# Kernel tuning notes

Hardware: AMD Instinct MI355X
Metric: run time of the kernel (lower is better)

The kernel has to match this reference:

```python
import jax, jax.numpy as jnp
import numpy as np

EPS = 1e-5

def _dw_conv_bn(x, w, gamma, beta):
    # depthwise 'same' conv: w is (C,1,k,k), feature_group_count = C
    C = x.shape[1]
    k = w.shape[-1]
    p = k // 2
    y = jax.lax.conv_general_dilated(
        x, w,
        window_strides=(1, 1),
        padding=((p, p), (p, p)),
        dimension_numbers=("NCHW", "OIHW", "NCHW"),
        feature_group_count=C,
    )
    # BatchNorm2d (training mode: batch stats over N,H,W per channel, biased var)
    mean = jnp.mean(y, axis=(0, 2, 3), keepdims=True)
    var = jnp.var(y, axis=(0, 2, 3), keepdims=True)
    inv = jax.lax.rsqrt(var + EPS)
    g = gamma.reshape(1, -1, 1, 1)
    b = beta.reshape(1, -1, 1, 1)
    return (y - mean) * inv * g + b


def setup_inputs() -> dict:
    key = jax.random.key(0)
    ks = jax.random.split(key, 3)
    B, C, H, W = 16, 384, 56, 56
    x = jax.random.normal(ks[0], (B, C, H, W), dtype=jnp.float32)
    w_large = jax.random.normal(ks[1], (C, 1, 31, 31), dtype=jnp.float32) * 0.02
    w_small = jax.random.normal(ks[2], (C, 1, 5, 5), dtype=jnp.float32) * 0.1
    gamma_large = jnp.ones((C,), dtype=jnp.float32)
    beta_large = jnp.zeros((C,), dtype=jnp.float32)
    gamma_small = jnp.ones((C,), dtype=jnp.float32)
    beta_small = jnp.zeros((C,), dtype=jnp.float32)
    return {
        "x": x,
        "w_large": w_large, "gamma_large": gamma_large, "beta_large": beta_large,
        "w_small": w_small, "gamma_small": gamma_small, "beta_small": beta_small,
    }


def reference(x, w_large, gamma_large, beta_large, w_small, gamma_small, beta_small):
    out = _dw_conv_bn(x, w_large, gamma_large, beta_large)
    out = out + _dw_conv_bn(x, w_small, gamma_small, beta_small)
    return out
```

## Files before the change

kernel.cpp:

```cpp
#include <hip/hip_runtime.h>
#include <hip/hip_bf16.h>

#define BB 16
#define CC 384
#define HH 56
#define WW 56
#define PLANE (HH*WW)
#define NHW (BB*PLANE)

typedef __attribute__((ext_vector_type(8)))  short short8;
typedef __attribute__((ext_vector_type(16))) float f32x16;
typedef __attribute__((ext_vector_type(4)))  unsigned int uint4v;
typedef __attribute__((ext_vector_type(4)))  float float4v;
typedef unsigned int uint;

#define PSTR 92
#define PROWS 86
#define PSZ (PROWS*PSTR)
#define WL_W 100
#define WS_W 80

static __device__ __forceinline__ short f2bf(float f) {
    unsigned int u = __float_as_uint(f);
    unsigned int r = (u + 0x7fffu + ((u >> 16) & 1u)) >> 16;
    return (short)r;
}

static __device__ __forceinline__ short8 ldA(const short* ap) {
    union { uint u[4]; short8 v; } r;
    uint2 lo = *(const uint2*)(ap);
    uint2 hi = *(const uint2*)(ap + 4);
    r.u[0] = lo.x; r.u[1] = lo.y; r.u[2] = hi.x; r.u[3] = hi.y;
    return r.v;
}

static __device__ __forceinline__ short8 ldW(const uint* p) {
    union { uint u[4]; short8 v; } r;
    r.u[0] = p[0]; r.u[1] = p[2]; r.u[2] = p[4]; r.u[3] = p[6];
    return r.v;
}

template<bool PACK>
__global__ __launch_bounds__(256)
__attribute__((amdgpu_waves_per_eu(3)))
void conv_large_k(
    const float* __restrict__ x, const float* __restrict__ wL,
    const float* __restrict__ wS,
    unsigned short* __restrict__ yL, uint* __restrict__ pk,
    float* __restrict__ stats)
{
    __shared__ __align__(16) short planes[2*PSZ];
    __shared__ __align__(16) uint  wpL[31*WL_W];
    __shared__ __align__(16) uint  wpS[5*WS_W];
    __shared__ float red_s[16];

    const int bid  = blockIdx.x;
    const int c    = bid % CC;
    const int pg   = bid / CC;
    const int tid  = threadIdx.x;
    const int w    = tid >> 6;
    const int p    = w >> 1;
    const int tx   = w & 1;
    const int lane = tid & 63;
    const int m    = lane & 31;
    const int g    = lane >> 5;

    {
        uint4 z = make_uint4(0,0,0,0);
        uint4* p4 = (uint4*)planes;
        #pragma unroll 1
        for (int i = tid; i < 2*PSZ/8; i += 256) p4[i] = z;
    }
    __syncthreads();

    short* pl = planes + p*PSZ;
    const int b = pg*2 + p;
    const float4* xp4 = (const float4*)(x + ((size_t)b*CC + c)*PLANE);
    #pragma unroll 1
    for (int i4 = lane + 64*tx; i4 < PLANE/4; i4 += 128) {
        float4 v = xp4[i4];
        int e  = 4*i4;
        int r  = e / WW;
        int cc = e - r*WW;
        short* dst = &pl[(r + 15)*PSTR + cc + 15];
        dst[0] = f2bf(v.x); dst[1] = f2bf(v.y); dst[2] = f2bf(v.z); dst[3] = f2bf(v.w);
    }

    const float* wrow = wL + c*961;
    #pragma unroll 1
    for (int i = tid; i < 31*WL_W; i += 256) {
        int ky = i / WL_W;
        int j  = i - ky*WL_W;
        int widx = j - 32;
        uint lo = (widx   >= 0 && widx   < 31) ? (uint)(unsigned short)f2bf(wrow[ky*31 + widx])     : 0u;
        uint hi = (widx+1 >= 0 && widx+1 < 31) ? (uint)(unsigned short)f2bf(wrow[ky*31 + widx + 1]) : 0u;
        wpL[i] = lo | (hi << 16);
    }
    const float* wrowS = wS + c*25;
    #pragma unroll 1
    for (int i = tid; i < 5*WS_W; i += 256) {
        int ky = i / WS_W;
        int j  = i - ky*WS_W;
        int widx = j - 32;
        uint lo = (widx   >= 0 && widx   < 5) ? (uint)(unsigned short)f2bf(wrowS[ky*5 + widx])     : 0u;
        uint hi = (widx+1 >= 0 && widx+1 < 5) ? (uint)(unsigned short)f2bf(wrowS[ky*5 + widx + 1]) : 0u;
        wpS[i] = lo | (hi << 16);
    }
    __syncthreads();

    const int  toff = 8*g - m;
    const uint* wLd = wpL + (toff + 32);
    const uint* wSd = wpS + (toff + 31);
    const short* abase = pl + m*PSTR + 8*g + tx*24;

    f32x16 acc[2] = {};

    short8 A0[8], B0[4], A1[8], B1[4];
    {
        #pragma unroll
        for (int s = 0; s < 4; ++s) B0[s] = ldW(wLd + 16*s);
        #pragma unroll
        for (int s = 0; s < 4; ++s) {
            A0[2*s]   = ldA(abase + 16*s);
            A0[2*s+1] = ldA(abase + 24*PSTR + 16*s);
        }
    }
    #pragma unroll 1
    for (int ky = 0; ky < 30; ky += 2) {
        {
            const uint* wk = wLd + (ky+1)*WL_W;
            const short* ar = abase + (ky+1)*PSTR;
            #pragma unroll
            for (int s = 0; s < 4; ++s) B1[s] = ldW(wk + 16*s);
            #pragma unroll
            for (int s = 0; s < 4; ++s) {
                A1[2*s]   = ldA(ar + 16*s);
                A1[2*s+1] = ldA(ar + 24*PSTR + 16*s);
            }
            #pragma unroll
            for (int s = 0; s < 4; ++s) {
                acc[0] = __builtin_amdgcn_mfma_f32_32x32x16_bf16(A0[2*s],   B0[s], acc[0], 0, 0, 0);
                acc[1] = __builtin_amdgcn_mfma_f32_32x32x16_bf16(A0[2*s+1], B0[s], acc[1], 0, 0, 0);
            }
        }
        {
            const uint* wk = wLd + (ky+2)*WL_W;
            const short* ar = abase + (ky+2)*PSTR;
            #pragma unroll
            for (int s = 0; s < 4; ++s) B0[s] = ldW(wk + 16*s);
            #pragma unroll
            for (int s = 0; s < 4; ++s) {
                A0[2*s]   = ldA(ar + 16*s);
                A0[2*s+1] = ldA(ar + 24*PSTR + 16*s);
            }
            #pragma unroll
            for (int s = 0; s < 4; ++s) {
                acc[0] = __builtin_amdgcn_mfma_f32_32x32x16_bf16(A1[2*s],   B1[s], acc[0], 0, 0, 0);
                acc[1] = __builtin_amdgcn_mfma_f32_32x32x16_bf16(A1[2*s+1], B1[s], acc[1], 0, 0, 0);
            }
        }
    }
    #pragma unroll
    for (int s = 0; s < 4; ++s) {
        acc[0] = __builtin_amdgcn_mfma_f32_32x32x16_bf16(A0[2*s],   B0[s], acc[0], 0, 0, 0);
        acc[1] = __builtin_amdgcn_mfma_f32_32x32x16_bf16(A0[2*s+1], B0[s], acc[1], 0, 0, 0);
    }

    float sL = 0.f, sL2 = 0.f, sS = 0.f, sS2 = 0.f;
    unsigned short* yout = yL + ((size_t)b*CC + c)*PLANE;
    uint*           pout = pk + ((size_t)b*CC + c)*PLANE;

    #pragma unroll
    for (int ty = 0; ty < 2; ++ty) {
        __builtin_amdgcn_sched_barrier(0);
        f32x16 aS_ = {};
        const short* asb = abase + (ty*24 + 13)*PSTR + 12;
        #pragma unroll 1
        for (int k2 = 0; k2 < 5; ++k2) {
            const uint* wk2 = wSd + k2*WS_W;
            const short* ar2 = asb + k2*PSTR;
            #pragma unroll
            for (int s = 0; s < 3; ++s) {
                short8 bs = ldW(wk2 + 16*s);
                short8 av = ldA(ar2 + 16*s);
                aS_ = __builtin_amdgcn_mfma_f32_32x32x16_bf16(av, bs, aS_, 0, 0, 0);
            }
        }
        const float cm = (tx == 0 || m >= 8) ? 1.f : 0.f;
        #pragma unroll
        for (int r = 0; r < 16; ++r) {
            float v  = acc[ty][r];
            float v2 = aS_[r];
            if (ty == 0 || r >= 4) {
                sL  = fmaf(cm, v,   sL);
                sL2 = fmaf(cm, v*v, sL2);
                sS  = fmaf(cm, v2,    sS);
                sS2 = fmaf(cm, v2*v2, sS2);
            }
            const int row = (r & 3) + 8*(r >> 2) + 4*g;
            const int ofs = (ty*24 + row)*WW + tx*24 + m;
            if (PACK) {
                pout[ofs] = (uint)(unsigned short)f2bf(v) | ((uint)(unsigned short)f2bf(v2) << 16);
            } else {
                yout[ofs] = (unsigned short)f2bf(v);
            }
        }
    }

    #pragma unroll
    for (int off = 32; off > 0; off >>= 1) {
        sL  += __shfl_down(sL,  off);
        sL2 += __shfl_down(sL2, off);
        sS  += __shfl_down(sS,  off);
        sS2 += __shfl_down(sS2, off);
    }
    if (lane == 0) {
        red_s[w*4 + 0] = sL;  red_s[w*4 + 1] = sL2;
        red_s[w*4 + 2] = sS;  red_s[w*4 + 3] = sS2;
    }
    __syncthreads();
    if (tid == 0) {
        float a = 0.f, e = 0.f, d0 = 0.f, e2 = 0.f;
        #pragma unroll
        for (int i = 0; i < 4; ++i) {
            a  += red_s[i*4 + 0]; e  += red_s[i*4 + 1];
            d0 += red_s[i*4 + 2]; e2 += red_s[i*4 + 3];
        }
        atomicAdd(&stats[c],        a);
        atomicAdd(&stats[CC + c],   e);
        atomicAdd(&stats[2*CC + c], d0);
        atomicAdd(&stats[3*CC + c], e2);
    }
}

__global__ __launch_bounds__(256) void fuse_pack_k(
    const uint* __restrict__ pk, const float* __restrict__ stats,
    const float* __restrict__ gL, const float* __restrict__ bL,
    const float* __restrict__ gS, const float* __restrict__ bS,
    float* __restrict__ out)
{
    const int bid = blockIdx.x;
    const int c   = bid % CC;
    const int tid = threadIdx.x;

    const uint4v* pp0 = (const uint4v*)(pk + (size_t)bid * PLANE);
    const uint4v* pp1 = (const uint4v*)(pk + ((size_t)bid + 3072) * PLANE);
    float4v* op0 = (float4v*)(out + (size_t)bid * PLANE);
    float4v* op1 = (float4v*)(out + ((size_t)bid + 3072) * PLANE);

    uint4v v0 = __builtin_nontemporal_load(pp0 + tid);
    uint4v v1 = __builtin_nontemporal_load(pp0 + tid + 256);
    uint4v v2 = __builtin_nontemporal_load(pp0 + tid + 512);
    uint4v v3 = __builtin_nontemporal_load(pp1 + tid);
    uint4v v4 = __builtin_nontemporal_load(pp1 + tid + 256);
    uint4v v5 = __builtin_nontemporal_load(pp1 + tid + 512);

    const float inv_n = 1.0f / (float)NHW;
    float mL = stats[c]          * inv_n;
    float vL = stats[CC + c]     * inv_n - mL * mL;
    float aL = rsqrtf(vL + 1e-5f) * gL[c];
    float mS = stats[2*CC + c]   * inv_n;
    float vS = stats[3*CC + c]   * inv_n - mS * mS;
    float aS = rsqrtf(vS + 1e-5f) * gS[c];
    float cst = bL[c] + bS[c] - mL * aL - mS * aS;

    #define AFF(u) fmaf(aL, __uint_as_float((u) << 16), fmaf(aS, __uint_as_float((u) & 0xffff0000u), cst))
    #define AFF4(dst, src) { float4v t_; t_[0]=AFF(src[0]); t_[1]=AFF(src[1]); t_[2]=AFF(src[2]); t_[3]=AFF(src[3]); dst = t_; }
    float4v r;
    AFF4(r, v0); __builtin_nontemporal_store(r, op0 + tid);
    AFF4(r, v1); __builtin_nontemporal_store(r, op0 + tid + 256);
    AFF4(r, v2); __builtin_nontemporal_store(r, op0 + tid + 512);
    AFF4(r, v3); __builtin_nontemporal_store(r, op1 + tid);
    AFF4(r, v4); __builtin_nontemporal_store(r, op1 + tid + 256);
    AFF4(r, v5); __builtin_nontemporal_store(r, op1 + tid + 512);
    if (tid < PLANE/4 - 768) {
        uint4v t0 = __builtin_nontemporal_load(pp0 + tid + 768);
        uint4v t1 = __builtin_nontemporal_load(pp1 + tid + 768);
        AFF4(r, t0); __builtin_nontemporal_store(r, op0 + tid + 768);
        AFF4(r, t1); __builtin_nontemporal_store(r, op1 + tid + 768);
    }
    #undef AFF4
    #undef AFF
}

#define ST3 61
__global__ __launch_bounds__(256) void fuse_small_k(
    const float* __restrict__ x, const float* __restrict__ wS,
    const unsigned short* __restrict__ yL, const float* __restrict__ stats,
    const float* __restrict__ gL, const float* __restrict__ bL,
    const float* __restrict__ gS, const float* __restrict__ bS,
    float* __restrict__ out)
{
    __shared__ float in_s[60 * ST3];

    const int bid = blockIdx.x;
    const int c   = bid % CC;
    const int tid = threadIdx.x;
    const float* __restrict__ w2 = wS + c * 25;

    for (int i = tid; i < 60 * ST3; i += 256) in_s[i] = 0.f;
    __syncthreads();

    const float4* xp4 = (const float4*)(x + (size_t)bid * PLANE);
    for (int t = tid; t < PLANE / 4; t += 256) {
        int r  = t / (WW / 4);
        int c4 = (t - r * (WW / 4)) * 4;
        float4 v = xp4[t];
        float* dst = &in_s[(r + 2) * ST3 + 2 + c4];
        dst[0] = v.x; dst[1] = v.y; dst[2] = v.z; dst[3] = v.w;
    }
    __syncthreads();

    const float inv_n = 1.0f / (float)NHW;
    float mL = stats[c]          * inv_n;
    float vL = stats[CC + c]     * inv_n - mL * mL;
    float aL = rsqrtf(vL + 1e-5f) * gL[c];
    float mS = stats[2*CC + c]   * inv_n;
    float vS = stats[3*CC + c]   * inv_n - mS * mS;
    float aS = rsqrtf(vS + 1e-5f) * gS[c];
    float cst = bL[c] + bS[c] - mL * aL - mS * aS;

    const unsigned short* yp = yL + (size_t)bid * PLANE;
    float* op = out + (size_t)bid * PLANE;

    #pragma unroll 1
    for (int t = tid; t < PLANE / 4; t += 256) {
        int r  = t / 14;
        int c4 = (t - r * 14) * 4;
        float o0 = 0.f, o1 = 0.f, o2 = 0.f, o3 = 0.f;
        #pragma unroll
        for (int ky = 0; ky < 5; ++ky) {
            const float* rp = &in_s[(r + ky) * ST3 + c4];
            float f[9];
            #pragma unroll
            for (int j = 0; j < 9; ++j) f[j] = rp[j];
            const float* wr = w2 + ky * 5;
            #pragma unroll
            for (int kx = 0; kx < 5; ++kx) {
                float wv = wr[kx];
                o0 = fmaf(f[kx + 0], wv, o0);
                o1 = fmaf(f[kx + 1], wv, o1);
                o2 = fmaf(f[kx + 2], wv, o2);
                o3 = fmaf(f[kx + 3], wv, o3);
            }
        }
        ushort4 yv = *(const ushort4*)(yp + 4 * t);
        float4 res;
        res.x = fmaf(aL, __uint_as_float(((uint)yv.x) << 16), fmaf(aS, o0, cst));
        res.y = fmaf(aL, __uint_as_float(((uint)yv.y) << 16), fmaf(aS, o1, cst));
        res.z = fmaf(aL, __uint_as_float(((uint)yv.z) << 16), fmaf(aS, o2, cst));
        res.w = fmaf(aL, __uint_as_float(((uint)yv.w) << 16), fmaf(aS, o3, cst));
        *(float4*)(op + 4 * t) = res;
    }
}

extern "C" void kernel_launch(void* const* d_in, const int* in_sizes, int n_in,
                              void* d_out, int out_size, void* d_ws, size_t ws_size,
                              hipStream_t stream) {
    const float* x  = (const float*)d_in[0];
    const float* wL = (const float*)d_in[1];
    const float* gL = (const float*)d_in[2];
    const float* bL = (const float*)d_in[3];
    const float* wS = (const float*)d_in[4];
    const float* gS = (const float*)d_in[5];
    const float* bS = (const float*)d_in[6];
    float* out = (float*)d_out;

    const size_t pk_bytes = (size_t)BB * CC * PLANE * sizeof(uint);
    const size_t yl_bytes = (size_t)BB * CC * PLANE * sizeof(unsigned short);
    const bool pack = ws_size >= pk_bytes + 4 * CC * sizeof(float);

    if (pack) {
        uint* pkbuf  = (uint*)d_ws;
        float* stats = (float*)((char*)d_ws + pk_bytes);
        hipMemsetAsync(stats, 0, 4 * CC * sizeof(float), stream);
        conv_large_k<true><<<8 * CC, 256, 0, stream>>>(x, wL, wS, (unsigned short*)d_ws, pkbuf, stats);
        fuse_pack_k<<<BB * CC / 2, 256, 0, stream>>>(pkbuf, stats, gL, bL, gS, bS, out);
    } else {
        unsigned short* yLbuf = (unsigned short*)d_ws;
        float* stats = (float*)((char*)d_ws + yl_bytes);
        hipMemsetAsync(stats, 0, 4 * CC * sizeof(float), stream);
        conv_large_k<false><<<8 * CC, 256, 0, stream>>>(x, wL, wS, yLbuf, (uint*)d_ws, stats);
        fuse_small_k<<<BB * CC, 256, 0, stream>>>(x, wS, yLbuf, stats, gL, bL, gS, bS, out);
    }
}
```

Before: 273.9 us.

## Fuse conv and BN-apply into persistent kernel with grid-wide barrier

Replaces the two-kernel pack path with one persistent kernel of 2*CC blocks. Each block loops over 8 batch images for a single channel, which lets it load the weights once and accumulate batch statistics locally. It then waits at an atomic-counter grid barrier and applies the BatchNorm affine to its own outputs, removing one launch and the gap between kernels. The barrier requires all 768 blocks to be co-resident, and a spin timeout guards against deadlock. The fallback conv kernel's software-pipelined inner loop is also simplified to a plain loop, but that path only runs when the workspace is too small.

```diff
diff --git a/kernel.cpp b/kernel.cpp
--- a/kernel.cpp
+++ b/kernel.cpp
@@ -38,6 +38,241 @@
     union { uint u[4]; short8 v; } r;
     r.u[0] = p[0]; r.u[1] = p[2]; r.u[2] = p[4]; r.u[3] = p[6];
     return r.v;
+}
+
+__global__ __launch_bounds__(256)
+__attribute__((amdgpu_waves_per_eu(3)))
+void fused_persist_k(
+    const float* __restrict__ x, const float* __restrict__ wL,
+    const float* __restrict__ wS, uint* __restrict__ pk,
+    float* __restrict__ stats, uint* __restrict__ ctr,
+    const float* __restrict__ gL, const float* __restrict__ bL,
+    const float* __restrict__ gS, const float* __restrict__ bS,
+    float* __restrict__ out)
+{
+    __shared__ __align__(16) short planes[2*PSZ];
+    __shared__ __align__(16) uint  wpL[31*WL_W];
+    __shared__ __align__(16) uint  wpS[5*WS_W];
+    __shared__ float red_s[16];
+
+    const int cp   = blockIdx.x;
+    const int c    = cp >> 1;
+    const int half = cp & 1;
+    const int tid  = threadIdx.x;
+    const int w    = tid >> 6;
+    const int p    = w >> 1;
+    const int tx   = w & 1;
+    const int lane = tid & 63;
+    const int m    = lane & 31;
+    const int g    = lane >> 5;
+
+    {
+        uint4 z = make_uint4(0,0,0,0);
+        uint4* p4 = (uint4*)planes;
+        #pragma unroll 1
+        for (int i = tid; i < 2*PSZ/8; i += 256) p4[i] = z;
+    }
+
+    const float* wrow = wL + c*961;
+    #pragma unroll 1
+    for (int i = tid; i < 31*WL_W; i += 256) {
+        int ky = i / WL_W;
+        int j  = i - ky*WL_W;
+        int widx = j - 32;
+        uint lo = (widx   >= 0 && widx   < 31) ? (uint)(unsigned short)f2bf(wrow[ky*31 + widx])     : 0u;
+        uint hi = (widx+1 >= 0 && widx+1 < 31) ? (uint)(unsigned short)f2bf(wrow[ky*31 + widx + 1]) : 0u;
+        wpL[i] = lo | (hi << 16);
+    }
+    const float* wrowS = wS + c*25;
+    #pragma unroll 1
+    for (int i = tid; i < 5*WS_W; i += 256) {
+        int ky = i / WS_W;
+        int j  = i - ky*WS_W;
+        int widx = j - 32;
+        uint lo = (widx   >= 0 && widx   < 5) ? (uint)(unsigned short)f2bf(wrowS[ky*5 + widx])     : 0u;
+        uint hi = (widx+1 >= 0 && widx+1 < 5) ? (uint)(unsigned short)f2bf(wrowS[ky*5 + widx + 1]) : 0u;
+        wpS[i] = lo | (hi << 16);
+    }
+
+    const int  toff = 8*g - m;
+    const uint* wLd = wpL + (toff + 32);
+    const uint* wSd = wpS + (toff + 31);
+    short* pl = planes + p*PSZ;
+    const short* abase = pl + m*PSTR + 8*g + tx*24;
+
+    float sL = 0.f, sL2 = 0.f, sS = 0.f, sS2 = 0.f;
+
+    #pragma unroll 1
+    for (int u = 0; u < 4; ++u) {
+        const int b = (half*4 + u)*2 + p;
+        __syncthreads();
+
+        const float4* xp4 = (const float4*)(x + ((size_t)b*CC + c)*PLANE);
+        #pragma unroll 1
+        for (int i4 = lane + 64*tx; i4 < PLANE/4; i4 += 128) {
+            float4 v = xp4[i4];
+            int e  = 4*i4;
+            int r  = e / WW;
+            int cc = e - r*WW;
+            short* dst = &pl[(r + 15)*PSTR + cc + 15];
+            dst[0] = f2bf(v.x); dst[1] = f2bf(v.y); dst[2] = f2bf(v.z); dst[3] = f2bf(v.w);
+        }
+        __syncthreads();
+
+        f32x16 acc[2] = {};
+
+        short8 A0[8], B0[4], A1[8], B1[4];
+        #pragma unroll
+        for (int s = 0; s < 4; ++s) B0[s] = ldW(wLd + 16*s);
+        #pragma unroll
+        for (int s = 0; s < 4; ++s) {
+            A0[2*s]   = ldA(abase + 16*s);
+            A0[2*s+1] = ldA(abase + 24*PSTR + 16*s);
+        }
+        #pragma unroll 1
+        for (int ky = 0; ky < 30; ky += 2) {
+            {
+                const uint* wk = wLd + (ky+1)*WL_W;
+                const short* ar = abase + (ky+1)*PSTR;
+                #pragma unroll
+                for (int s = 0; s < 4; ++s) B1[s] = ldW(wk + 16*s);
+                #pragma unroll
+                for (int s = 0; s < 4; ++s) {
+                    A1[2*s]   = ldA(ar + 16*s);
+                    A1[2*s+1] = ldA(ar + 24*PSTR + 16*s);
+                }
+                #pragma unroll
+                for (int s = 0; s < 4; ++s) {
+                    acc[0] = __builtin_amdgcn_mfma_f32_32x32x16_bf16(A0[2*s],   B0[s], acc[0], 0, 0, 0);
+                    acc[1] = __builtin_amdgcn_mfma_f32_32x32x16_bf16(A0[2*s+1], B0[s], acc[1], 0, 0, 0);
+                }
+            }
+            {
+                const uint* wk = wLd + (ky+2)*WL_W;
+                const short* ar = abase + (ky+2)*PSTR;
+                #pragma unroll
+                for (int s = 0; s < 4; ++s) B0[s] = ldW(wk + 16*s);
+                #pragma unroll
+                for (int s = 0; s < 4; ++s) {
+                    A0[2*s]   = ldA(ar + 16*s);
+                    A0[2*s+1] = ldA(ar + 24*PSTR + 16*s);
+                }
+                #pragma unroll
+                for (int s = 0; s < 4; ++s) {
+                    acc[0] = __builtin_amdgcn_mfma_f32_32x32x16_bf16(A1[2*s],   B1[s], acc[0], 0, 0, 0);
+                    acc[1] = __builtin_amdgcn_mfma_f32_32x32x16_bf16(A1[2*s+1], B1[s], acc[1], 0, 0, 0);
+                }
+            }
+        }
+        #pragma unroll
+        for (int s = 0; s < 4; ++s) {
+            acc[0] = __builtin_amdgcn_mfma_f32_32x32x16_bf16(A0[2*s],   B0[s], acc[0], 0, 0, 0);
+            acc[1] = __builtin_amdgcn_mfma_f32_32x32x16_bf16(A0[2*s+1], B0[s], acc[1], 0, 0, 0);
+        }
+
+        uint* pout = pk + ((size_t)b*CC + c)*PLANE;
+        #pragma unroll
+        for (int ty = 0; ty < 2; ++ty) {
+            __builtin_amdgcn_sched_barrier(0);
+            f32x16 aS_ = {};
+            const short* asb = abase + (ty*24 + 13)*PSTR + 12;
+            #pragma unroll 1
+            for (int k2 = 0; k2 < 5; ++k2) {
+                const uint* wk2 = wSd + k2*WS_W;
+                const short* ar2 = asb + k2*PSTR;
+                #pragma unroll
+                for (int s = 0; s < 3; ++s) {
+                    short8 bs = ldW(wk2 + 16*s);
+                    short8 av = ldA(ar2 + 16*s);
+                    aS_ = __builtin_amdgcn_mfma_f32_32x32x16_bf16(av, bs, aS_, 0, 0, 0);
+                }
+            }
+            const float cm = (tx == 0 || m >= 8) ? 1.f : 0.f;
+            #pragma unroll
+            for (int r = 0; r < 16; ++r) {
+                float v  = acc[ty][r];
+                float v2 = aS_[r];
+                if (ty == 0 || r >= 4) {
+                    sL  = fmaf(cm, v,   sL);
+                    sL2 = fmaf(cm, v*v, sL2);
+                    sS  = fmaf(cm, v2,    sS);
+                    sS2 = fmaf(cm, v2*v2, sS2);
+                }
+                const int row = (r & 3) + 8*(r >> 2) + 4*g;
+                const int ofs = (ty*24 + row)*WW + tx*24 + m;
+                pout[ofs] = (uint)(unsigned short)f2bf(v) | ((uint)(unsigned short)f2bf(v2) << 16);
+            }
+        }
+    }
+
+    #pragma unroll
+    for (int off = 32; off > 0; off >>= 1) {
+        sL  += __shfl_down(sL,  off);
+        sL2 += __shfl_down(sL2, off);
+        sS  += __shfl_down(sS,  off);
+        sS2 += __shfl_down(sS2, off);
+    }
+    if (lane == 0) {
+        red_s[w*4 + 0] = sL;  red_s[w*4 + 1] = sL2;
+        red_s[w*4 + 2] = sS;  red_s[w*4 + 3] = sS2;
+    }
+    __syncthreads();
+    if (tid == 0) {
+        float a = 0.f, e = 0.f, d0 = 0.f, e2 = 0.f;
+        #pragma unroll
+        for (int i = 0; i < 4; ++i) {
+            a  += red_s[i*4 + 0]; e  += red_s[i*4 + 1];
+            d0 += red_s[i*4 + 2]; e2 += red_s[i*4 + 3];
+        }
+        atomicAdd(&stats[c],        a);
+        atomicAdd(&stats[CC + c],   e);
+        atomicAdd(&stats[2*CC + c], d0);
+        atomicAdd(&stats[3*CC + c], e2);
+
+        __threadfence();
+        atomicAdd(ctr, 1u);
+        uint spins = 0;
+        while (__hip_atomic_load(ctr, __ATOMIC_ACQUIRE, __HIP_MEMORY_SCOPE_AGENT) < (uint)gridDim.x) {
+            __builtin_amdgcn_s_sleep(2);
+            if (++spins > 100000000u) break;
+        }
+    }
+    __syncthreads();
+
+    const float inv_n = 1.0f / (float)NHW;
+    float s0 = __hip_atomic_load(&stats[c],        __ATOMIC_RELAXED, __HIP_MEMORY_SCOPE_AGENT);
+    float s1 = __hip_atomic_load(&stats[CC + c],   __ATOMIC_RELAXED, __HIP_MEMORY_SCOPE_AGENT);
+    float s2 = __hip_atomic_load(&stats[2*CC + c], __ATOMIC_RELAXED, __HIP_MEMORY_SCOPE_AGENT);
+    float s3 = __hip_atomic_load(&stats[3*CC + c], __ATOMIC_RELAXED, __HIP_MEMORY_SCOPE_AGENT);
+    float mL = s0 * inv_n;
+    float vL = s1 * inv_n - mL * mL;
+    float aL = rsqrtf(vL + 1e-5f) * gL[c];
+    float mS = s2 * inv_n;
+    float vS = s3 * inv_n - mS * mS;
+    float aS = rsqrtf(vS + 1e-5f) * gS[c];
+    float cst = bL[c] + bS[c] - mL * aL - mS * aS;
+
+    #define AFF(u) fmaf(aL, __uint_as_float((u) << 16), fmaf(aS, __uint_as_float((u) & 0xffff0000u), cst))
+    #define AFF4(dst, src) { float4v t_; t_[0]=AFF(src[0]); t_[1]=AFF(src[1]); t_[2]=AFF(src[2]); t_[3]=AFF(src[3]); dst = t_; }
+    #pragma unroll 1
+    for (int j = 0; j < 8; ++j) {
+        const size_t bj = ((size_t)(half*8 + j)*CC + c)*(size_t)PLANE;
+        const uint4v* pp = (const uint4v*)(pk + bj);
+        float4v*      op = (float4v*)(out + bj);
+        uint4v v0 = pp[tid];
+        uint4v v1 = pp[tid + 256];
+        uint4v v2 = pp[tid + 512];
+        float4v r;
+        AFF4(r, v0); op[tid]       = r;
+        AFF4(r, v1); op[tid + 256] = r;
+        AFF4(r, v2); op[tid + 512] = r;
+        if (tid < PLANE/4 - 768) {
+            uint4v v3 = pp[tid + 768];
+            AFF4(r, v3); op[tid + 768] = r;
+        }
+    }
+    #undef AFF4
+    #undef AFF
 }
 
 template<bool PACK>
@@ -115,55 +350,20 @@
 
     f32x16 acc[2] = {};
 
-    short8 A0[8], B0[4], A1[8], B1[4];
-    {
-        #pragma unroll
-        for (int s = 0; s < 4; ++s) B0[s] = ldW(wLd + 16*s);
+    #pragma unroll 1
+    for (int ky = 0; ky < 31; ++ky) {
+        const uint* wk = wLd + ky*WL_W;
+        short8 Bv[4];
+        #pragma unroll
+        for (int s = 0; s < 4; ++s) Bv[s] = ldW(wk + 16*s);
+        const short* ar = abase + ky*PSTR;
         #pragma unroll
         for (int s = 0; s < 4; ++s) {
-            A0[2*s]   = ldA(abase + 16*s);
-            A0[2*s+1] = ldA(abase + 24*PSTR + 16*s);
-        }
-    }
-    #pragma unroll 1
-    for (int ky = 0; ky < 30; ky += 2) {
-        {
-            const uint* wk = wLd + (ky+1)*WL_W;
-            const short* ar = abase + (ky+1)*PSTR;
-            #pragma unroll
-            for (int s = 0; s < 4; ++s) B1[s] = ldW(wk + 16*s);
-            #pragma unroll
-            for (int s = 0; s < 4; ++s) {
-                A1[2*s]   = ldA(ar + 16*s);
-                A1[2*s+1] = ldA(ar + 24*PSTR + 16*s);
-            }
-            #pragma unroll
-            for (int s = 0; s < 4; ++s) {
-                acc[0] = __builtin_amdgcn_mfma_f32_32x32x16_bf16(A0[2*s],   B0[s], acc[0], 0, 0, 0);
-                acc[1] = __builtin_amdgcn_mfma_f32_32x32x16_bf16(A0[2*s+1], B0[s], acc[1], 0, 0, 0);
-            }
-        }
-        {
-            const uint* wk = wLd + (ky+2)*WL_W;
-            const short* ar = abase + (ky+2)*PSTR;
-            #pragma unroll
-            for (int s = 0; s < 4; ++s) B0[s] = ldW(wk + 16*s);
-            #pragma unroll
-            for (int s = 0; s < 4; ++s) {
-                A0[2*s]   = ldA(ar + 16*s);
-                A0[2*s+1] = ldA(ar + 24*PSTR + 16*s);
-            }
-            #pragma unroll
-            for (int s = 0; s < 4; ++s) {
-                acc[0] = __builtin_amdgcn_mfma_f32_32x32x16_bf16(A1[2*s],   B1[s], acc[0], 0, 0, 0);
-                acc[1] = __builtin_amdgcn_mfma_f32_32x32x16_bf16(A1[2*s+1], B1[s], acc[1], 0, 0, 0);
-            }
-        }
-    }
-    #pragma unroll
-    for (int s = 0; s < 4; ++s) {
-        acc[0] = __builtin_amdgcn_mfma_f32_32x32x16_bf16(A0[2*s],   B0[s], acc[0], 0, 0, 0);
-        acc[1] = __builtin_amdgcn_mfma_f32_32x32x16_bf16(A0[2*s+1], B0[s], acc[1], 0, 0, 0);
+            short8 A0 = ldA(ar + 16*s);
+            short8 A1 = ldA(ar + 24*PSTR + 16*s);
+            acc[0] = __builtin_amdgcn_mfma_f32_32x32x16_bf16(A0, Bv[s], acc[0], 0, 0, 0);
+            acc[1] = __builtin_amdgcn_mfma_f32_32x32x16_bf16(A1, Bv[s], acc[1], 0, 0, 0);
+        }
     }
 
     float sL = 0.f, sL2 = 0.f, sS = 0.f, sS2 = 0.f;
@@ -233,56 +433,6 @@
     }
 }
 
-__global__ __launch_bounds__(256) void fuse_pack_k(
-    const uint* __restrict__ pk, const float* __restrict__ stats,
-    const float* __restrict__ gL, const float* __restrict__ bL,
-    const float* __restrict__ gS, const float* __restrict__ bS,
-    float* __restrict__ out)
-{
-    const int bid = blockIdx.x;
-    const int c   = bid % CC;
-    const int tid = threadIdx.x;
-
-    const uint4v* pp0 = (const uint4v*)(pk + (size_t)bid * PLANE);
-    const uint4v* pp1 = (const uint4v*)(pk + ((size_t)bid + 3072) * PLANE);
-    float4v* op0 = (float4v*)(out + (size_t)bid * PLANE);
-    float4v* op1 = (float4v*)(out + ((size_t)bid + 3072) * PLANE);
-
-    uint4v v0 = __builtin_nontemporal_load(pp0 + tid);
-    uint4v v1 = __builtin_nontemporal_load(pp0 + tid + 256);
-    uint4v v2 = __builtin_nontemporal_load(pp0 + tid + 512);
-    uint4v v3 = __builtin_nontemporal_load(pp1 + tid);
-    uint4v v4 = __builtin_nontemporal_load(pp1 + tid + 256);
-    uint4v v5 = __builtin_nontemporal_load(pp1 + tid + 512);
-
-    const float inv_n = 1.0f / (float)NHW;
-    float mL = stats[c]          * inv_n;
-    float vL = stats[CC + c]     * inv_n - mL * mL;
-    float aL = rsqrtf(vL + 1e-5f) * gL[c];
-    float mS = stats[2*CC + c]   * inv_n;
-    float vS = stats[3*CC + c]   * inv_n - mS * mS;
-    float aS = rsqrtf(vS + 1e-5f) * gS[c];
-    float cst = bL[c] + bS[c] - mL * aL - mS * aS;
-
-    #define AFF(u) fmaf(aL, __uint_as_float((u) << 16), fmaf(aS, __uint_as_float((u) & 0xffff0000u), cst))
-    #define AFF4(dst, src) { float4v t_; t_[0]=AFF(src[0]); t_[1]=AFF(src[1]); t_[2]=AFF(src[2]); t_[3]=AFF(src[3]); dst = t_; }
-    float4v r;
-    AFF4(r, v0); __builtin_nontemporal_store(r, op0 + tid);
-    AFF4(r, v1); __builtin_nontemporal_store(r, op0 + tid + 256);
-    AFF4(r, v2); __builtin_nontemporal_store(r, op0 + tid + 512);
-    AFF4(r, v3); __builtin_nontemporal_store(r, op1 + tid);
-    AFF4(r, v4); __builtin_nontemporal_store(r, op1 + tid + 256);
-    AFF4(r, v5); __builtin_nontemporal_store(r, op1 + tid + 512);
-    if (tid < PLANE/4 - 768) {
-        uint4v t0 = __builtin_nontemporal_load(pp0 + tid + 768);
-        uint4v t1 = __builtin_nontemporal_load(pp1 + tid + 768);
-        AFF4(r, t0); __builtin_nontemporal_store(r, op0 + tid + 768);
-        AFF4(r, t1); __builtin_nontemporal_store(r, op1 + tid + 768);
-    }
-    #undef AFF4
-    #undef AFF
-}
-
 #define ST3 61
 __global__ __launch_bounds__(256) void fuse_small_k(
     const float* __restrict__ x, const float* __restrict__ wS,
@@ -368,14 +518,15 @@
 
     const size_t pk_bytes = (size_t)BB * CC * PLANE * sizeof(uint);
     const size_t yl_bytes = (size_t)BB * CC * PLANE * sizeof(unsigned short);
-    const bool pack = ws_size >= pk_bytes + 4 * CC * sizeof(float);
+    const bool pack = ws_size >= pk_bytes + 4 * CC * sizeof(float) + 16;
 
     if (pack) {
         uint* pkbuf  = (uint*)d_ws;
         float* stats = (float*)((char*)d_ws + pk_bytes);
-        hipMemsetAsync(stats, 0, 4 * CC * sizeof(float), stream);
-        conv_large_k<true><<<8 * CC, 256, 0, stream>>>(x, wL, wS, (unsigned short*)d_ws, pkbuf, stats);
-        fuse_pack_k<<<BB * CC / 2, 256, 0, stream>>>(pkbuf, stats, gL, bL, gS, bS, out);
+        uint*  ctr   = (uint*)(stats + 4 * CC);
+        hipMemsetAsync(stats, 0, 4 * CC * sizeof(float) + 16, stream);
+        fused_persist_k<<<2 * CC, 256, 0, stream>>>(x, wL, wS, pkbuf, stats, ctr,
+                                                    gL, bL, gS, bS, out);
     } else {
         unsigned short* yLbuf = (unsigned short*)d_ws;
         float* stats = (float*)((char*)d_ws + yl_bytes);
```

After: 394.7 us. 1.44x slower.
